# Kernel tuning notes

Hardware: AMD Instinct MI355X
Metric: run time of the kernel (lower is better)

The kernel has to match this reference:

```python
import jax, jax.numpy as jnp
import numpy as np

ENSEMBLE_MAX_MEAN = 0.5  # weight on max-pooled similarity
EPS = 1e-12


def _l2norm(x, axis):
    return x / jnp.sqrt(jnp.sum(x * x, axis=axis, keepdims=True) + EPS)


def setup_inputs() -> dict:
    key = jax.random.key(0)
    k1, k2 = jax.random.split(key)
    image_feat = jax.random.normal(k1, (8, 512, 32, 32), dtype=jnp.float32)  # [B,C,H,W]
    proto_emb = jax.random.normal(k2, (150, 32, 512), dtype=jnp.float32)    # [N,K,C]
    return {"image_feat": image_feat, "proto_emb": proto_emb}


def reference(image_feat, proto_emb):
    # cosine similarity branch of FreeDAMasker.forward_seg
    # image_feat: [B,C,H,W], proto_emb: [N,K,C]
    img = _l2norm(image_feat, axis=1)
    pro = _l2norm(proto_emb, axis=-1)
    # simmap: [B,N,K,H,W]
    simmap = jnp.einsum('bchw,nkc->bnkhw', img, pro)
    sim_max = jnp.max(simmap, axis=2)   # [B,N,H,W]
    sim_mean = jnp.mean(simmap, axis=2)  # [B,N,H,W]
    sim = ENSEMBLE_MAX_MEAN * sim_max + (1.0 - ENSEMBLE_MAX_MEAN) * sim_mean
    # sim2mask: deterministic=True, hard=False -> soft sigmoid mask
    soft_mask = jax.nn.sigmoid(sim)
    return soft_mask, sim
```

## Files before the change

kernel.cpp:

```cpp
#include <hip/hip_runtime.h>
#include <hip/hip_bf16.h>

#define NPROT 150
#define KPROT 32
#define CDIM  512
#define BDIM  8
#define HWDIM 1024
#define MDIM  (NPROT * KPROT)
#define PDIM  (BDIM * HWDIM)

typedef int i32x4 __attribute__((ext_vector_type(4)));

#define QSA 508.0f
#define QSB 24.0f
#define DEQAB (1.0f / (508.0f * 24.0f))

__device__ __forceinline__ int q8a(float x) {
  return __float2int_rn(fminf(fmaxf(x * QSA, -127.0f), 127.0f));
}
__device__ __forceinline__ int q8b(float x) {
  return __float2int_rn(fminf(fmaxf(x * QSB, -127.0f), 127.0f));
}
__device__ __forceinline__ unsigned int pack4(int a, int b, int c, int d) {
  return (unsigned int)((a & 255) | ((b & 255) << 8) | ((c & 255) << 16) | ((d & 255) << 24));
}

#define GLOAD_LDS16(gsrc, ldst) __builtin_amdgcn_global_load_lds(            \
    (const __attribute__((address_space(1))) void*)(gsrc),                   \
    (__attribute__((address_space(3))) void*)(ldst), 16, 0, 0)

__global__ __launch_bounds__(256) void prep_k(const float* __restrict__ img,
                                              const float* __restrict__ proto,
                                              char* __restrict__ Ai8,
                                              char* __restrict__ Bi8,
                                              float* __restrict__ invB) {
  __shared__ char tile[32][528];
  __shared__ float psum[8][32];
  int t   = threadIdx.x;
  int bid = blockIdx.x;
  if (bid >= 256) {
    int row  = (bid - 256) * 4 + (t >> 6);
    int lane = t & 63;
    const float4* rp = (const float4*)(proto + (size_t)row * CDIM);
    float4 v0 = rp[lane * 2];
    float4 v1 = rp[lane * 2 + 1];
    float ss = v0.x*v0.x + v0.y*v0.y + v0.z*v0.z + v0.w*v0.w
             + v1.x*v1.x + v1.y*v1.y + v1.z*v1.z + v1.w*v1.w;
    #pragma unroll
    for (int o = 32; o > 0; o >>= 1) ss += __shfl_xor(ss, o, 64);
    float inv = rsqrtf(ss + 1e-12f);
    uint2 o8;
    o8.x = pack4(q8a(v0.x*inv), q8a(v0.y*inv), q8a(v0.z*inv), q8a(v0.w*inv));
    o8.y = pack4(q8a(v1.x*inv), q8a(v1.y*inv), q8a(v1.z*inv), q8a(v1.w*inv));
    *(uint2*)(Ai8 + (size_t)row * CDIM + lane * 8) = o8;
    return;
  }
  int b   = bid >> 5;
  int hw0 = (bid & 31) << 5;
  int hwo = t & 31;
  int cg  = t >> 5;
  const float* base = img + ((size_t)b << 19) + hw0 + hwo;
  float ss = 0.f;
  #pragma unroll 4
  for (int i = 0; i < 64; i += 4) {
    int c = cg * 64 + i;
    float x0 = base[(size_t)(c + 0) << 10];
    float x1 = base[(size_t)(c + 1) << 10];
    float x2 = base[(size_t)(c + 2) << 10];
    float x3 = base[(size_t)(c + 3) << 10];
    ss += x0*x0 + x1*x1 + x2*x2 + x3*x3;
    *(unsigned int*)&tile[hwo][c] = pack4(q8b(x0), q8b(x1), q8b(x2), q8b(x3));
  }
  psum[cg][hwo] = ss;
  __syncthreads();
  if (t < 32) {
    float s = 0.f;
    #pragma unroll
    for (int j = 0; j < 8; ++j) s += psum[j][t];
    invB[((size_t)b << 10) + hw0 + t] = rsqrtf(s + 1e-12f);
  }
  #pragma unroll
  for (int it = 0; it < 4; ++it) {
    int gi  = it * 256 + t;
    int pix = gi >> 5, gr = gi & 31;
    int4 v = *(const int4*)&tile[pix][gr * 16];
    *(int4*)(Bi8 + (((size_t)b << 10) + hw0 + pix) * CDIM + gr * 16) = v;
  }
}

__global__ __launch_bounds__(256, 4) void gemm_k(const char* __restrict__ Ai8,
                                                 const char* __restrict__ Bi8,
                                                 const float* __restrict__ invB,
                                                 float* __restrict__ out) {
  __shared__ __align__(16) char smem[(128 + 128) * 128];
  char* As = smem;
  char* Bs = smem + 128 * 128;

  int t    = threadIdx.x;
  int lane = t & 63;
  int w    = t >> 6;
  int wm   = w >> 1;
  int wp   = w & 1;
  int lr   = lane & 15;
  int lg   = lane >> 4;

  int bid = blockIdx.x;
  int xcd = bid & 7;
  int idx = bid >> 3;
  int bp  = (xcd << 3) + idx / 38;
  int bm  = idx % 38;
  int m0  = bm * 128;
  int p0  = bp * 128;

  i32x4 acc[4][4] = {};

  const char* Bb = Bi8 + (size_t)p0 * CDIM;

  for (int c0 = 0; c0 < CDIM; c0 += 128) {
    #pragma unroll
    for (int it = 0; it < 4; ++it) {
      int gi  = it * 256 + t;
      int row = gi >> 3, g = gi & 7;
      int gs  = g ^ (row & 7);
      int grow = m0 + row; grow = grow < MDIM ? grow : (MDIM - 1);
      GLOAD_LDS16(Ai8 + (size_t)grow * CDIM + c0 + gs * 16, As + gi * 16);
    }
    #pragma unroll
    for (int it = 0; it < 4; ++it) {
      int gi  = it * 256 + t;
      int row = gi >> 3, g = gi & 7;
      int gs  = g ^ (row & 7);
      GLOAD_LDS16(Bb + (size_t)row * CDIM + c0 + gs * 16, Bs + gi * 16);
    }
    __syncthreads();

    #pragma unroll
    for (int ks = 0; ks < 2; ++ks) {
      int gbase = ks * 4 + lg;
      i32x4 a4[4], b4[4];
      #pragma unroll
      for (int f = 0; f < 4; ++f) {
        int row = wm * 64 + f * 16 + lr;
        a4[f] = *(const i32x4*)(As + row * 128 + (gbase ^ (row & 7)) * 16);
      }
      #pragma unroll
      for (int f = 0; f < 4; ++f) {
        int row = wp * 64 + f * 16 + lr;
        b4[f] = *(const i32x4*)(Bs + row * 128 + (gbase ^ (row & 7)) * 16);
      }
      #pragma unroll
      for (int fm = 0; fm < 4; ++fm)
        #pragma unroll
        for (int fp = 0; fp < 4; ++fp)
          acc[fm][fp] = __builtin_amdgcn_mfma_i32_16x16x64_i8(a4[fm], b4[fp], acc[fm][fp], 0, 0, 0);
    }
    __syncthreads();
  }

  #pragma unroll
  for (int gi2 = 0; gi2 < 2; ++gi2) {
    #pragma unroll
    for (int fp = 0; fp < 4; ++fp) {
      float mx = -1e30f, sm = 0.f;
      #pragma unroll
      for (int fm = 2 * gi2; fm < 2 * gi2 + 2; ++fm)
        #pragma unroll
        for (int r = 0; r < 4; ++r) {
          float v = (float)acc[fm][fp][r];
          mx = fmaxf(mx, v);
          sm += v;
        }
      mx = fmaxf(mx, __shfl_xor(mx, 16, 64));
      mx = fmaxf(mx, __shfl_xor(mx, 32, 64));
      sm += __shfl_xor(sm, 16, 64);
      sm += __shfl_xor(sm, 32, 64);
      if (lg == 0) {
        int n = bm * 4 + wm * 2 + gi2;
        if (n < NPROT) {
          int p  = p0 + wp * 64 + fp * 16 + lr;
          float scale = DEQAB * invB[p];
          float sim   = (0.5f * mx + sm * (0.5f / 32.0f)) * scale;
          float mask  = 1.0f / (1.0f + __expf(-sim));
          int b  = p >> 10, hw = p & 1023;
          size_t o = ((size_t)(b * NPROT + n) << 10) + hw;
          out[o] = mask;
          out[(size_t)(BDIM * NPROT * HWDIM) + o] = sim;
        }
      }
    }
  }
}

extern "C" void kernel_launch(void* const* d_in, const int* in_sizes, int n_in,
                              void* d_out, int out_size, void* d_ws, size_t ws_size,
                              hipStream_t stream) {
  const float* img   = (const float*)d_in[0];
  const float* proto = (const float*)d_in[1];
  float* out = (float*)d_out;
  char*  Ai8  = (char*)d_ws;
  char*  Bi8  = Ai8 + (size_t)MDIM * CDIM;
  float* invB = (float*)(Bi8 + (size_t)PDIM * CDIM);

  prep_k<<<256 + MDIM / 4, 256, 0, stream>>>(img, proto, Ai8, Bi8, invB);
  gemm_k<<<2432, 256, 0, stream>>>(Ai8, Bi8, invB, out);
}
```

Baseline: 41.89 us.

## Double-buffer int8 GEMM LDS tiles with 64-wide K stages and prefetch

The GEMM main loop moves from a single-buffered 128-wide K tile to two 16KB LDS buffers holding 64-wide K slices. The next slice is prefetched with global_load_lds while MFMAs run on the current one, using explicit vmcnt waits and barriers, and the swizzle is adjusted for 64-byte rows. MFMA sections get raised scheduling priority. Total LDS stays at 32KB, but the number of K iterations and barriers doubles.

```diff
diff --git a/kernel.cpp b/kernel.cpp
--- a/kernel.cpp
+++ b/kernel.cpp
@@ -92,9 +92,7 @@
                                                  const char* __restrict__ Bi8,
                                                  const float* __restrict__ invB,
                                                  float* __restrict__ out) {
-  __shared__ __align__(16) char smem[(128 + 128) * 128];
-  char* As = smem;
-  char* Bs = smem + 128 * 128;
+  __shared__ __align__(16) char smem[2 * 16384];
 
   int t    = threadIdx.x;
   int lane = t & 63;
@@ -112,50 +110,74 @@
   int m0  = bm * 128;
   int p0  = bp * 128;
 
+  const char* Bb = Bi8 + (size_t)p0 * CDIM;
+
+  int aoff[4], boff[4];
+  #pragma unroll
+  for (int f = 0; f < 4; ++f) {
+    int ra = wm * 64 + f * 16 + lr;
+    aoff[f] = ra * 64 + ((lg ^ ((ra >> 1) & 3)) << 4);
+    int rb = wp * 64 + f * 16 + lr;
+    boff[f] = 8192 + rb * 64 + ((lg ^ ((rb >> 1) & 3)) << 4);
+  }
+
   i32x4 acc[4][4] = {};
 
-  const char* Bb = Bi8 + (size_t)p0 * CDIM;
-
-  for (int c0 = 0; c0 < CDIM; c0 += 128) {
-    #pragma unroll
-    for (int it = 0; it < 4; ++it) {
-      int gi  = it * 256 + t;
-      int row = gi >> 3, g = gi & 7;
-      int gs  = g ^ (row & 7);
-      int grow = m0 + row; grow = grow < MDIM ? grow : (MDIM - 1);
-      GLOAD_LDS16(Ai8 + (size_t)grow * CDIM + c0 + gs * 16, As + gi * 16);
-    }
-    #pragma unroll
-    for (int it = 0; it < 4; ++it) {
-      int gi  = it * 256 + t;
-      int row = gi >> 3, g = gi & 7;
-      int gs  = g ^ (row & 7);
-      GLOAD_LDS16(Bb + (size_t)row * CDIM + c0 + gs * 16, Bs + gi * 16);
-    }
-    __syncthreads();
-
-    #pragma unroll
-    for (int ks = 0; ks < 2; ++ks) {
-      int gbase = ks * 4 + lg;
-      i32x4 a4[4], b4[4];
-      #pragma unroll
-      for (int f = 0; f < 4; ++f) {
-        int row = wm * 64 + f * 16 + lr;
-        a4[f] = *(const i32x4*)(As + row * 128 + (gbase ^ (row & 7)) * 16);
-      }
-      #pragma unroll
-      for (int f = 0; f < 4; ++f) {
-        int row = wp * 64 + f * 16 + lr;
-        b4[f] = *(const i32x4*)(Bs + row * 128 + (gbase ^ (row & 7)) * 16);
-      }
-      #pragma unroll
-      for (int fm = 0; fm < 4; ++fm)
-        #pragma unroll
-        for (int fp = 0; fp < 4; ++fp)
-          acc[fm][fp] = __builtin_amdgcn_mfma_i32_16x16x64_i8(a4[fm], b4[fp], acc[fm][fp], 0, 0, 0);
-    }
-    __syncthreads();
-  }
+#define STAGE(S) do {                                                         \
+    const int buf_ = (S) & 1; const int cb_ = (S) * 64;                       \
+    _Pragma("unroll")                                                         \
+    for (int it = 0; it < 2; ++it) {            \
+      int gi = it * 256 + t, row = gi >> 2, g = gi & 3;                       \
+      int gs = g ^ ((row >> 1) & 3);                                          \
+      int grow = m0 + row; grow = grow < MDIM ? grow : (MDIM - 1);            \
+      GLOAD_LDS16(Ai8 + (size_t)grow * CDIM + cb_ + gs * 16,                  \
+                  smem + buf_ * 16384 + gi * 16);                             \
+    }                                                                         \
+    _Pragma("unroll")                                                         \
+    for (int it = 0; it < 2; ++it) {            \
+      int gi = it * 256 + t, row = gi >> 2, g = gi & 3;                       \
+      int gs = g ^ ((row >> 1) & 3);                                          \
+      GLOAD_LDS16(Bb + (size_t)row * CDIM + cb_ + gs * 16,                    \
+                  smem + buf_ * 16384 + 8192 + gi * 16);                      \
+    }                                                                         \
+    __builtin_amdgcn_sched_barrier(0);                                        \
+  } while (0)
+
+#define WAITV(N) { asm volatile("s_waitcnt vmcnt(" #N ")" ::: "memory");      \
+                   __builtin_amdgcn_sched_barrier(0); }
+#define BAR() { __builtin_amdgcn_sched_barrier(0);                            \
+                __builtin_amdgcn_s_barrier();                                 \
+                __builtin_amdgcn_sched_barrier(0); }
+
+#define COMPUTE(S) do {                                                       \
+    const char* base_ = smem + ((S) & 1) * 16384;                             \
+    i32x4 a4[4], b4[4];                                                       \
+    _Pragma("unroll")                                                         \
+    for (int f = 0; f < 4; ++f) a4[f] = *(const i32x4*)(base_ + aoff[f]);     \
+    _Pragma("unroll")                                                         \
+    for (int f = 0; f < 4; ++f) b4[f] = *(const i32x4*)(base_ + boff[f]);     \
+    __builtin_amdgcn_s_setprio(1);                                            \
+    _Pragma("unroll")                                                         \
+    for (int fm = 0; fm < 4; ++fm)                                            \
+      _Pragma("unroll")                                                       \
+      for (int fp = 0; fp < 4; ++fp)                                          \
+        acc[fm][fp] = __builtin_amdgcn_mfma_i32_16x16x64_i8(                  \
+            a4[fm], b4[fp], acc[fm][fp], 0, 0, 0);                            \
+    __builtin_amdgcn_s_setprio(0);                                            \
+  } while (0)
+
+  STAGE(0);
+  #pragma unroll
+  for (int s = 0; s < 7; ++s) {
+    STAGE(s + 1);
+    WAITV(4);
+    BAR();
+    COMPUTE(s);
+    BAR();
+  }
+  WAITV(0);
+  BAR();
+  COMPUTE(7);
 
   #pragma unroll
   for (int gi2 = 0; gi2 < 2; ++gi2) {
@@ -189,6 +211,10 @@
       }
     }
   }
+#undef STAGE
+#undef WAITV
+#undef BAR
+#undef COMPUTE
 }
 
 extern "C" void kernel_launch(void* const* d_in, const int* in_sizes, int n_in,
```

After: 40.89 us, median of 2. 2.4% less time.
